# Kernel optimization log

Measured on AMD Instinct MI355X. Metric: run time of the kernel, lower is better.

Reference implementation:

```python
import jax, jax.numpy as jnp
import numpy as np

NUM_HEAD = 8
EMBED_DIM = 512


def setup_inputs() -> dict:
    key = jax.random.key(0)
    ks = jax.random.split(key, 9)
    B, N, D = 4, 2048, 512
    # xavier_uniform bound for square [D, D] weights
    bound = float(np.sqrt(6.0 / (D + EMBED_DIM)))
    return {
        "q": jax.random.normal(ks[0], (B, N, D), jnp.float32),
        "k": jax.random.normal(ks[1], (B, N, D), jnp.float32),
        "v": jax.random.normal(ks[2], (B, N, D), jnp.float32),
        "Wq": jax.random.uniform(ks[3], (D, EMBED_DIM), jnp.float32, -bound, bound),
        "Wk": jax.random.uniform(ks[4], (D, EMBED_DIM), jnp.float32, -bound, bound),
        "Wv": jax.random.uniform(ks[5], (D, EMBED_DIM), jnp.float32, -bound, bound),
        "bq": jnp.zeros((EMBED_DIM,), jnp.float32),
        "bk": jnp.zeros((EMBED_DIM,), jnp.float32),
        "bv": jnp.zeros((EMBED_DIM,), jnp.float32),
    }


def reference(q, k, v, Wq, Wk, Wv, bq, bk, bv):
    h = NUM_HEAD
    ch = EMBED_DIM // h
    B, N, _ = q.shape
    # linear projections
    Q = q @ Wq + bq  # [B, N, E]
    K = k @ Wk + bk
    V = v @ Wv + bv
    # split heads: b n (h ch) -> b h n ch
    Q = Q.reshape(B, N, h, ch).transpose(0, 2, 1, 3)
    K = K.reshape(B, N, h, ch).transpose(0, 2, 1, 3)
    V = V.reshape(B, N, h, ch).transpose(0, 2, 1, 3)
    scale = 1.0 / np.sqrt(ch).astype(np.float32)
    scores = jnp.einsum("bhqc,bhkc->bhqk", Q, K) * scale  # [B, h, N, N]
    attn = jax.nn.softmax(scores, axis=-1)
    out = jnp.einsum("bhqk,bhkc->bhqc", attn, V)  # [B, h, N, ch]
    # merge heads: b h n ch -> b n (h ch)
    return out.transpose(0, 2, 1, 3).reshape(B, N, EMBED_DIM)
```

## Files before the change

### kernel.cpp

```cpp
#include <hip/hip_runtime.h>
#include <hip/hip_bf16.h>
#include <cstdint>

#define B_ 4
#define N_ 2048
#define D_ 512
#define E_ 512
#define H_ 8
#define CH_ 64
#define M_ (B_*N_)

typedef __attribute__((ext_vector_type(8))) short bf16x8;
typedef __attribute__((ext_vector_type(4))) float f32x4;
typedef __attribute__((ext_vector_type(16))) float f32x16;
using u16 = unsigned short;
using u32 = unsigned int;

__device__ __forceinline__ u16 f2bf(float f) {
  union { __hip_bfloat16 h; u16 u; } cv;
  cv.h = __float2bfloat16(f);
  return cv.u;
}

__device__ __forceinline__ float fexp2(float x) {
#if __has_builtin(__builtin_amdgcn_exp2f)
  return __builtin_amdgcn_exp2f(x);
#else
  return exp2f(x);
#endif
}

__device__ __forceinline__ void async16(const void* g, void* l) {
  __builtin_amdgcn_global_load_lds(
      (__attribute__((address_space(1))) void*)(g),
      (__attribute__((address_space(3))) void*)(l),
      16, 0, 0);
}

__global__ void prep(const float* __restrict__ q, const float* __restrict__ k,
                     const float* __restrict__ v,
                     const float* __restrict__ Wq, const float* __restrict__ Wk,
                     const float* __restrict__ Wv,
                     u16* __restrict__ qb, u16* __restrict__ kb, u16* __restrict__ vb,
                     u16* __restrict__ tq, u16* __restrict__ tk, u16* __restrict__ tv) {
  int bid = blockIdx.x;
  if (bid < 12288) {
    int t = bid >> 12;
    const float* in = (t == 0) ? q : (t == 1 ? k : v);
    u16* outp = (t == 0) ? qb : (t == 1 ? kb : vb);
    int i = ((bid & 4095) << 8) + threadIdx.x;
    float4 f = reinterpret_cast<const float4*>(in)[i];
    ushort4 o;
    o.x = f2bf(f.x); o.y = f2bf(f.y); o.z = f2bf(f.z); o.w = f2bf(f.w);
    reinterpret_cast<ushort4*>(outp)[i] = o;
  } else {
    bid -= 12288;
    int t = bid >> 10;
    const float* W = (t == 0) ? Wq : (t == 1 ? Wk : Wv);
    u16* T = (t == 0) ? tq : (t == 1 ? tk : tv);
    int idx = ((bid & 1023) << 8) + threadIdx.x;
    int e = idx >> 9, kd = idx & 511;
    T[idx] = f2bf(W[kd * E_ + e]);
  }
}

#define GBM 128
#define GBN 64
#define GBK 64

__global__ __launch_bounds__(256) void proj_gemm(
    const u16* __restrict__ xq, const u16* __restrict__ xk, const u16* __restrict__ xv,
    const u16* __restrict__ wtq, const u16* __restrict__ wtk, const u16* __restrict__ wtv,
    const float* __restrict__ bq, const float* __restrict__ bk, const float* __restrict__ bv,
    u16* __restrict__ Qp, u16* __restrict__ Kp, u16* __restrict__ Vp) {
  const int bid = blockIdx.x;
  const int xcd = bid & 7;
  const int t   = bid >> 3;
  const int x8  = t & 7;
  const int gp  = xcd * 24 + (t >> 3);
  const int y   = gp & 63;
  const int z   = gp >> 6;

  const u16* X  = (z == 0) ? xq : (z == 1 ? xk : xv);
  const u16* WT = (z == 0) ? wtq : (z == 1 ? wtk : wtv);
  const float* bias = (z == 0) ? bq : (z == 1 ? bk : bv);
  u16* Out = (z == 0) ? Qp : (z == 1 ? Kp : Vp);
  const float scale = (z == 0) ? 0.18033688011112042f : 1.0f;
  const bool vlayout = (z == 2);

  __shared__ __align__(16) u16 As[GBM * GBK];
  __shared__ __align__(16) u16 Bs[GBN * GBK];

  const int tid = threadIdx.x;
  const int l = tid & 63, w = tid >> 6;
  const int wr = w >> 1, wc = w & 1;
  const int m0 = y * GBM;
  const int e0 = x8 * GBN;

  f32x4 acc[4][2] = {};

  for (int ks = 0; ks < D_ / GBK; ++ks) {
    const int k0 = ks * GBK;
#pragma unroll
    for (int i = 0; i < 4; ++i) {
      int o = i * 4096 + tid * 16;
      int row = o >> 7, colb = o & 127;
      int scol = colb ^ ((row & 7) << 4);
      async16((const char*)X + ((size_t)(m0 + row) * D_ + k0) * 2 + scol, (char*)As + o);
    }
#pragma unroll
    for (int i = 0; i < 2; ++i) {
      int o = i * 4096 + tid * 16;
      int row = o >> 7, colb = o & 127;
      int scol = colb ^ ((row & 7) << 4);
      async16((const char*)WT + ((size_t)(e0 + row) * D_ + k0) * 2 + scol, (char*)Bs + o);
    }
    __syncthreads();
#pragma unroll
    for (int kk = 0; kk < 2; ++kk) {
      bf16x8 af[4], bfr[2];
#pragma unroll
      for (int m = 0; m < 4; ++m) {
        int row = wr * 64 + m * 16 + (l & 15);
        int addr = (row << 7) + kk * 64 + ((l >> 4) << 4);
        addr ^= (row & 7) << 4;
        af[m] = *reinterpret_cast<const bf16x8*>((const char*)As + addr);
      }
#pragma unroll
      for (int n = 0; n < 2; ++n) {
        int row = wc * 32 + n * 16 + (l & 15);
        int addr = (row << 7) + kk * 64 + ((l >> 4) << 4);
        addr ^= (row & 7) << 4;
        bfr[n] = *reinterpret_cast<const bf16x8*>((const char*)Bs + addr);
      }
#pragma unroll
      for (int m = 0; m < 4; ++m)
#pragma unroll
        for (int n = 0; n < 2; ++n)
          acc[m][n] = __builtin_amdgcn_mfma_f32_16x16x32_bf16(af[m], bfr[n], acc[m][n], 0, 0, 0);
    }
    __syncthreads();
  }

#pragma unroll
  for (int m = 0; m < 4; ++m) {
#pragma unroll
    for (int n = 0; n < 2; ++n) {
      int ge = e0 + wc * 32 + n * 16 + (l & 15);
      int h = ge >> 6, c = ge & 63;
      float bv_ = bias[ge];
      int gm0 = m0 + wr * 64 + m * 16 + ((l >> 4) << 2);
      int b = gm0 >> 11, nn0 = gm0 & 2047;
      if (vlayout) {
        short4 sv;
#pragma unroll
        for (int j = 0; j < 4; ++j)
          ((u16*)&sv)[j] = f2bf((acc[m][n][j] + bv_) * scale);
        int np = (((nn0 >> 2) ^ (nn0 >> 3)) & 1) ? (nn0 ^ 12) : nn0;
        *reinterpret_cast<short4*>(
            &Out[(((size_t)b * H_ + h) * CH_ + c) * N_ + np]) = sv;
      } else {
#pragma unroll
        for (int j = 0; j < 4; ++j) {
          u16 oval = f2bf((acc[m][n][j] + bv_) * scale);
          Out[((((size_t)b * H_ + h) * N_ + nn0 + j) << 6) + c] = oval;
        }
      }
    }
  }
}

#define QBLK 128
#define KVB 32
#define NTH 32

#define MFMA32(A, Bv, C) __builtin_amdgcn_mfma_f32_32x32x16_bf16((A), (Bv), (C), 0, 0, 0)

__global__ __launch_bounds__(512, 2) void attn_kernel(
    const u16* __restrict__ Qp, const u16* __restrict__ Kp, const u16* __restrict__ Vp,
    float* __restrict__ out) {
  __shared__ __align__(16) u16 Kb[2][2][2048];
  __shared__ __align__(16) u16 Vb[2][2][2048];
  __shared__ float shL[4][64];

  const int tid = threadIdx.x;
  const int l = tid & 63, w = tid >> 6;
  const int wsub = w & 3, hf = w >> 2;
  const int qcol = l & 31, hi = l >> 5;

  const int beta = blockIdx.x;
  const int xcd = beta & 7, r = beta >> 3;
  const int bh = xcd * 4 + (r >> 4);
  const int qt = r & 15;

  const u16* Qh = Qp + (size_t)bh * N_ * CH_;
  const u16* Kh = Kp + (size_t)bh * N_ * CH_;
  const u16* Vh = Vp + (size_t)bh * CH_ * N_;
  const int bb = bh >> 3, hh = bh & 7;
  const int qrow = qt * QBLK + wsub * 32 + qcol;

  bf16x8 qf[4];
  {
    const u16* qptr = Qh + (size_t)qrow * CH_;
#pragma unroll
    for (int ks = 0; ks < 4; ++ks)
      qf[ks] = *reinterpret_cast<const bf16x8*>(qptr + ks * 16 + hi * 8);
  }

  f32x16 o0 = {}, o1 = {};
  float lrun = 0.f;

  const int kbase = ((qcol >> 1) << 8) + ((qcol & 1) << 4);
  const int kxor  = (qcol >> 1) & 7;
  const int vbase = ((qcol >> 2) << 8) + ((qcol & 3) << 4);
  const int vxor  = (qcol >> 2) & 3;

  const int st = tid & 255;
  const int tb = hf * (N_ / 2);

  const int so    = st * 16;
  const int kpair = so >> 8;
  const int krow  = (kpair << 1) | ((so >> 4) & 1);
  const int kcol  = ((((so >> 5) & 7) ^ (kpair & 7)) << 4) | (so & 15);
  const int vquad = so >> 8;
  const int vrow  = (vquad << 2) | ((so >> 4) & 3);
  const int vcol  = ((((so >> 6) & 3) ^ (vquad & 3)) << 4) | (so & 15);

#define STAGE(BUF, KV) do {                                                      \
    async16((const char*)Kh + (size_t)((KV) + krow) * 128 + kcol,                \
            (char*)&Kb[BUF][hf][0] + so);                                        \
    async16((const char*)Vh + (size_t)vrow * (N_ * 2) + (KV) * 2 + vcol,         \
            (char*)&Vb[BUF][hf][0] + so);                                        \
  } while (0)

#define TILE(BUF, TL) do {                                                       \
    if ((TL) + 1 < NTH) STAGE((BUF) ^ 1, tb + ((TL) + 1) * KVB);                 \
    f32x16 s0 = {};                                                              \
    __builtin_amdgcn_s_setprio(1);                                               \
    _Pragma("unroll")                                                            \
    for (int ks = 0; ks < 4; ++ks) {                                             \
      int ka = kbase + ((((ks << 1) | hi) ^ kxor) << 5);                         \
      bf16x8 kf = *reinterpret_cast<const bf16x8*>((const char*)&Kb[BUF][hf][0] + ka); \
      s0 = MFMA32(kf, qf[ks], s0);                                               \
    }                                                                            \
    __builtin_amdgcn_s_setprio(0);                                               \
    _Pragma("unroll")                                                            \
    for (int rr = 0; rr < 16; ++rr) s0[rr] = fexp2(s0[rr]);                      \
    {                                                                            \
      float t0 = (s0[0] + s0[1]) + (s0[2] + s0[3]);                              \
      float t1 = (s0[4] + s0[5]) + (s0[6] + s0[7]);                              \
      float t2 = (s0[8] + s0[9]) + (s0[10] + s0[11]);                            \
      float t3 = (s0[12] + s0[13]) + (s0[14] + s0[15]);                          \
      float rsum = (t0 + t1) + (t2 + t3);                                        \
      rsum += __shfl_xor(rsum, 32);                                              \
      lrun += rsum;                                                              \
    }                                                                            \
    __builtin_amdgcn_s_setprio(1);                                               \
    _Pragma("unroll")                                                            \
    for (int ks = 0; ks < 2; ++ks) {                                             \
      union { u16 us[8]; bf16x8 v8; } pu;                                        \
      _Pragma("unroll")                                                          \
      for (int j = 0; j < 8; ++j) pu.us[j] = f2bf(s0[ks * 8 + j]);               \
      int va = vbase + ((((ks << 1) | hi) ^ vxor) << 6);                         \
      bf16x8 v0 = *reinterpret_cast<const bf16x8*>((const char*)&Vb[BUF][hf][0] + va);        \
      bf16x8 v1 = *reinterpret_cast<const bf16x8*>((const char*)&Vb[BUF][hf][0] + va + 2048); \
      o0 = MFMA32(v0, pu.v8, o0);                                                \
      o1 = MFMA32(v1, pu.v8, o1);                                                \
    }                                                                            \
    __builtin_amdgcn_s_setprio(0);                                               \
    __syncthreads();                                                             \
  } while (0)

  STAGE(0, tb);
  __syncthreads();

  for (int tl = 0; tl < NTH; tl += 2) {
    TILE(0, tl);
    TILE(1, tl + 1);
  }

  float* pb = (wsub < 2) ? ((float*)&Kb[0][0][0] + wsub * 2048 + l * 4)
                         : ((float*)&Vb[0][0][0] + (wsub - 2) * 2048 + l * 4);
  if (hf == 1) {
#pragma unroll
    for (int c = 0; c < 4; ++c) {
      float4 s;
      s.x = o0[c * 4 + 0]; s.y = o0[c * 4 + 1];
      s.z = o0[c * 4 + 2]; s.w = o0[c * 4 + 3];
      *reinterpret_cast<float4*>(pb + c * 256) = s;
    }
#pragma unroll
    for (int c = 0; c < 4; ++c) {
      float4 s;
      s.x = o1[c * 4 + 0]; s.y = o1[c * 4 + 1];
      s.z = o1[c * 4 + 2]; s.w = o1[c * 4 + 3];
      *reinterpret_cast<float4*>(pb + (4 + c) * 256) = s;
    }
    shL[wsub][l] = lrun;
  }
  __syncthreads();
  if (hf == 0) {
    float inv = 1.0f / (lrun + shL[wsub][l]);
    const size_t obase = ((size_t)bb * N_ + qrow) * E_ + hh * CH_;
#pragma unroll
    for (int c = 0; c < 4; ++c) {
      float4 p = *reinterpret_cast<const float4*>(pb + c * 256);
      float4 stv;
      stv.x = (o0[c * 4 + 0] + p.x) * inv;
      stv.y = (o0[c * 4 + 1] + p.y) * inv;
      stv.z = (o0[c * 4 + 2] + p.z) * inv;
      stv.w = (o0[c * 4 + 3] + p.w) * inv;
      *reinterpret_cast<float4*>(out + obase + c * 8 + hi * 4) = stv;
    }
#pragma unroll
    for (int c = 0; c < 4; ++c) {
      float4 p = *reinterpret_cast<const float4*>(pb + (4 + c) * 256);
      float4 stv;
      stv.x = (o1[c * 4 + 0] + p.x) * inv;
      stv.y = (o1[c * 4 + 1] + p.y) * inv;
      stv.z = (o1[c * 4 + 2] + p.z) * inv;
      stv.w = (o1[c * 4 + 3] + p.w) * inv;
      *reinterpret_cast<float4*>(out + obase + 32 + c * 8 + hi * 4) = stv;
    }
  }
#undef STAGE
#undef TILE
}

extern "C" void kernel_launch(void* const* d_in, const int* in_sizes, int n_in,
                              void* d_out, int out_size, void* d_ws, size_t ws_size,
                              hipStream_t stream) {
  const float* q  = (const float*)d_in[0];
  const float* k  = (const float*)d_in[1];
  const float* v  = (const float*)d_in[2];
  const float* Wq = (const float*)d_in[3];
  const float* Wk = (const float*)d_in[4];
  const float* Wv = (const float*)d_in[5];
  const float* bq = (const float*)d_in[6];
  const float* bk = (const float*)d_in[7];
  const float* bv = (const float*)d_in[8];
  float* out = (float*)d_out;

  u16* wtq = (u16*)d_ws;
  u16* wtk = wtq + (size_t)D_ * E_;
  u16* wtv = wtk + (size_t)D_ * E_;
  u16* Qp  = wtv + (size_t)D_ * E_;
  u16* Kp  = Qp + (size_t)M_ * E_;
  u16* Vp  = Kp + (size_t)M_ * E_;
  u16* qb  = Vp + (size_t)M_ * E_;
  u16* kb  = qb + (size_t)M_ * D_;
  u16* vb  = kb + (size_t)M_ * D_;

  prep<<<15360, 256, 0, stream>>>(q, k, v, Wq, Wk, Wv, qb, kb, vb, wtq, wtk, wtv);
  proj_gemm<<<1536, 256, 0, stream>>>(
      qb, kb, vb, wtq, wtk, wtv, bq, bk, bv, Qp, Kp, Vp);
  attn_kernel<<<512, 512, 0, stream>>>(Qp, Kp, Vp, out);
}
```

Measured before the change: 79.87 us.

## Software-pipeline attention loop with 4-deep LDS ring and QK/PV overlap

Replaces the double-buffered K/V staging with a 4-slot LDS ring that prefetches three tiles ahead. Each step runs the QK MFMA for the next tile before the softmax and PV of the previous one, so exp and convert work can overlap with matrix ops. Explicit vmcnt waits and raw barriers replace __syncthreads, and the setprio hints are dropped. Launch bounds now ask for 4 blocks per CU, which limits registers per thread, while LDS use doubles and two score accumulators stay live at once, so occupancy and spills could get worse.

```diff
diff --git a/kernel.cpp b/kernel.cpp
--- a/kernel.cpp
+++ b/kernel.cpp
@@ -176,11 +176,11 @@
 
 #define MFMA32(A, Bv, C) __builtin_amdgcn_mfma_f32_32x32x16_bf16((A), (Bv), (C), 0, 0, 0)
 
-__global__ __launch_bounds__(512, 2) void attn_kernel(
+__global__ __launch_bounds__(512, 4) void attn_kernel(
     const u16* __restrict__ Qp, const u16* __restrict__ Kp, const u16* __restrict__ Vp,
     float* __restrict__ out) {
-  __shared__ __align__(16) u16 Kb[2][2][2048];
-  __shared__ __align__(16) u16 Vb[2][2][2048];
+  __shared__ __align__(16) u16 Kb[4][2][2048];
+  __shared__ __align__(16) u16 Vb[4][2][2048];
   __shared__ float shL[4][64];
 
   const int tid = threadIdx.x;
@@ -208,6 +208,7 @@
   }
 
   f32x16 o0 = {}, o1 = {};
+  f32x16 s_a = {}, s_b = {};
   float lrun = 0.f;
 
   const int kbase = ((qcol >> 1) << 8) + ((qcol & 1) << 4);
@@ -226,6 +227,12 @@
   const int vrow  = (vquad << 2) | ((so >> 4) & 3);
   const int vcol  = ((((so >> 6) & 3) ^ (vquad & 3)) << 4) | (so & 15);
 
+#define VM2  asm volatile("s_waitcnt vmcnt(2)" ::: "memory")
+#define VM0  asm volatile("s_waitcnt vmcnt(0)" ::: "memory")
+#define VM4  asm volatile("s_waitcnt vmcnt(4)" ::: "memory")
+#define BAR  do { __builtin_amdgcn_s_barrier(); \
+                  asm volatile("" ::: "memory"); } while (0)
+
 #define STAGE(BUF, KV) do {                                                      \
     async16((const char*)Kh + (size_t)((KV) + krow) * 128 + kcol,                \
             (char*)&Kb[BUF][hf][0] + so);                                        \
@@ -233,52 +240,60 @@
             (char*)&Vb[BUF][hf][0] + so);                                        \
   } while (0)
 
-#define TILE(BUF, TL) do {                                                       \
-    if ((TL) + 1 < NTH) STAGE((BUF) ^ 1, tb + ((TL) + 1) * KVB);                 \
-    f32x16 s0 = {};                                                              \
-    __builtin_amdgcn_s_setprio(1);                                               \
+#define QK(BUF, SD) do {                                                         \
     _Pragma("unroll")                                                            \
     for (int ks = 0; ks < 4; ++ks) {                                             \
       int ka = kbase + ((((ks << 1) | hi) ^ kxor) << 5);                         \
       bf16x8 kf = *reinterpret_cast<const bf16x8*>((const char*)&Kb[BUF][hf][0] + ka); \
-      s0 = MFMA32(kf, qf[ks], s0);                                               \
-    }                                                                            \
-    __builtin_amdgcn_s_setprio(0);                                               \
+      SD = MFMA32(kf, qf[ks], ks == 0 ? (f32x16){} : SD);                        \
+    } } while (0)
+
+#define SMPV(SIN, BUF) do {                                                      \
     _Pragma("unroll")                                                            \
-    for (int rr = 0; rr < 16; ++rr) s0[rr] = fexp2(s0[rr]);                      \
+    for (int rr = 0; rr < 16; ++rr) SIN[rr] = fexp2(SIN[rr]);                    \
     {                                                                            \
-      float t0 = (s0[0] + s0[1]) + (s0[2] + s0[3]);                              \
-      float t1 = (s0[4] + s0[5]) + (s0[6] + s0[7]);                              \
-      float t2 = (s0[8] + s0[9]) + (s0[10] + s0[11]);                            \
-      float t3 = (s0[12] + s0[13]) + (s0[14] + s0[15]);                          \
+      float t0 = (SIN[0] + SIN[1]) + (SIN[2] + SIN[3]);                          \
+      float t1 = (SIN[4] + SIN[5]) + (SIN[6] + SIN[7]);                          \
+      float t2 = (SIN[8] + SIN[9]) + (SIN[10] + SIN[11]);                        \
+      float t3 = (SIN[12] + SIN[13]) + (SIN[14] + SIN[15]);                      \
       float rsum = (t0 + t1) + (t2 + t3);                                        \
       rsum += __shfl_xor(rsum, 32);                                              \
       lrun += rsum;                                                              \
     }                                                                            \
-    __builtin_amdgcn_s_setprio(1);                                               \
     _Pragma("unroll")                                                            \
     for (int ks = 0; ks < 2; ++ks) {                                             \
       union { u16 us[8]; bf16x8 v8; } pu;                                        \
       _Pragma("unroll")                                                          \
-      for (int j = 0; j < 8; ++j) pu.us[j] = f2bf(s0[ks * 8 + j]);               \
+      for (int j = 0; j < 8; ++j) pu.us[j] = f2bf(SIN[ks * 8 + j]);              \
       int va = vbase + ((((ks << 1) | hi) ^ vxor) << 6);                         \
       bf16x8 v0 = *reinterpret_cast<const bf16x8*>((const char*)&Vb[BUF][hf][0] + va);        \
       bf16x8 v1 = *reinterpret_cast<const bf16x8*>((const char*)&Vb[BUF][hf][0] + va + 2048); \
       o0 = MFMA32(v0, pu.v8, o0);                                                \
       o1 = MFMA32(v1, pu.v8, o1);                                                \
-    }                                                                            \
-    __builtin_amdgcn_s_setprio(0);                                               \
-    __syncthreads();                                                             \
-  } while (0)
+    } } while (0)
 
   STAGE(0, tb);
+  STAGE(1, tb + KVB);
+  STAGE(2, tb + 2 * KVB);
+  VM4;
+  BAR;
+  QK(0, s_a);
+
+#define BODY(BQK, BPV, BST, SIN, SOUT, TST)                                      \
+  do { VM2; BAR; STAGE(BST, tb + (TST) * KVB); QK(BQK, SOUT); SMPV(SIN, BPV); } while (0)
+
+  for (int tt = 0; tt < NTH - 4; tt += 4) {
+    BODY(1, 0, 3, s_a, s_b, tt + 3);
+    BODY(2, 1, 0, s_b, s_a, tt + 4);
+    BODY(3, 2, 1, s_a, s_b, tt + 5);
+    BODY(0, 3, 2, s_b, s_a, tt + 6);
+  }
+  { VM2; BAR; STAGE(3, tb + (NTH - 1) * KVB); QK(1, s_b); SMPV(s_a, 0); }
+  { VM2; BAR;                                 QK(2, s_a); SMPV(s_b, 1); }
+  { VM0; BAR;                                 QK(3, s_b); SMPV(s_a, 2); }
+  { BAR;                                                  SMPV(s_b, 3); }
+
   __syncthreads();
-
-  for (int tl = 0; tl < NTH; tl += 2) {
-    TILE(0, tl);
-    TILE(1, tl + 1);
-  }
-
   float* pb = (wsub < 2) ? ((float*)&Kb[0][0][0] + wsub * 2048 + l * 4)
                          : ((float*)&Vb[0][0][0] + (wsub - 2) * 2048 + l * 4);
   if (hf == 1) {
@@ -324,7 +339,9 @@
     }
   }
 #undef STAGE
-#undef TILE
+#undef QK
+#undef SMPV
+#undef BODY
 }
 
 extern "C" void kernel_launch(void* const* d_in, const int* in_sizes, int n_in,
```

After: 94.88 us. 1.19x slower.
